# Performance work log

Hardware: AMD Instinct MI355X
Metric: run time of the kernel (lower is better)

The kernel has to match this reference:

```python
import jax, jax.numpy as jnp
import numpy as np

M = 30000      # total nodes
D = 64         # hidden_channels
B = 256        # number of graphs
E = 480000     # number of edges
NUM_ITER = 3   # Newton-Schulz iterations
EPS_TRIU = 0.001  # fix_triu diagonal jitter


def setup_inputs() -> dict:
    key = jax.random.key(0)
    k1, k2, k3 = jax.random.split(key, 3)
    x = jax.random.normal(k1, (M, D), dtype=jnp.float32)
    # sorted segment ids, every graph non-empty (sorted_randint semantics)
    batch = ((jnp.arange(M) * B) // M).astype(jnp.int32)
    edge = jax.random.randint(k2, (2, E), 0, M)
    W_att = jax.random.normal(k3, (D * D, 1), dtype=jnp.float32) / D
    b_att = jnp.zeros((1,), dtype=jnp.float32)
    return {"x": x, "batch": batch, "edge": edge, "W_att": W_att, "b_att": b_att}


def _segment_softmax(v, seg, num_segments):
    # v: [M], seg: [M] -> per-segment softmax
    m = jax.ops.segment_max(v, seg, num_segments=num_segments)
    e = jnp.exp(v - m[seg])
    s = jax.ops.segment_sum(e, seg, num_segments=num_segments)
    return e / s[seg]


def _sqrtm_ns(A, n_iter):
    # Newton-Schulz iterative matrix square root (MPN-COV Sqrtm)
    d = A.shape[-1]
    I = jnp.eye(d, dtype=A.dtype)
    normA = jnp.trace(A, axis1=-2, axis2=-1)[:, None, None]  # [B,1,1]
    Y = A / normA
    Z = jnp.broadcast_to(I, A.shape)
    for _ in range(n_iter):
        T = 0.5 * (3.0 * I - jnp.matmul(Z, Y))
        Y = jnp.matmul(Y, T)
        Z = jnp.matmul(T, Z)
    return Y * jnp.sqrt(normA)


def reference(x, batch, edge, W_att, b_att):
    Mn, Dd = x.shape
    # per-node outer products: einsum 'ik,kj->kij' on (x^T, x)
    wj = x[:, :, None] * x[:, None, :]              # [M, D, D]
    flat = wj.reshape(Mn, Dd * Dd)                  # [M, D*D]
    imp = (flat @ W_att + b_att)[:, 0]              # [M]
    imp = _segment_softmax(imp, batch, B)[:, None]  # scatter_softmax
    # scatter_mean(imp * flat, batch)
    num = jax.ops.segment_sum(imp * flat, batch, num_segments=B)
    cnt = jax.ops.segment_sum(jnp.ones((Mn,), x.dtype), batch, num_segments=B)
    out = (num / jnp.maximum(cnt, 1.0)[:, None]).reshape(B, Dd, Dd)
    # fix_triu: add eps * I before matrix sqrt
    out = out + EPS_TRIU * jnp.eye(Dd, dtype=out.dtype)
    out = _sqrtm_ns(out, NUM_ITER)
    # Triuvec: upper triangle incl. diagonal
    iu, ju = jnp.triu_indices(Dd)
    out = out[:, iu, ju]                            # [B, D*(D+1)/2]
    return out.reshape(B, -1)
```

## Files before the change

### kernel.cpp

```cpp
#include <hip/hip_runtime.h>
#include <math.h>

#define MN       30000
#define BSEG     256
#define EPS_TRIU 0.001f

#define XR_H 0
#define XR_L 8192
#define XT_H 16384
#define XT_L 24576
#define WT_H 32768
#define WT_L 36864
#define P_H 0
#define P_L 4096
#define Q_H 8192
#define Q_L 12288
#define R_H 16384
#define R_L 20480
#define S_H 24576
#define S_L 28672
#define V_H 32768
#define V_L 36864
#define IMP_F 20480
#define SWG_F 20608
#define SCL_F 20736
#define LDS_F4 5185

typedef __attribute__((ext_vector_type(8))) short bf16x8;
typedef __attribute__((ext_vector_type(4))) float f32x4;
#define MFMA_BF16(a, b, c) __builtin_amdgcn_mfma_f32_16x16x32_bf16(a, b, c, 0, 0, 0)

__device__ __forceinline__ float bf2f(short s) {
  return __uint_as_float(((unsigned)(unsigned short)s) << 16);
}
__device__ __forceinline__ void split2(float val, unsigned short& h, unsigned short& l) {
  const unsigned u = __float_as_uint(val);
  h = (unsigned short)(u >> 16);
  const float lo = val - __uint_as_float(u & 0xFFFF0000u);
  l = (unsigned short)(__float_as_uint(lo) >> 16);
}
__device__ __forceinline__ int sw64(int r, int c) { return (r << 6) + (c ^ ((r & 7) << 3)); }
__device__ __forceinline__ int sw128(int r, int c) { return (r << 7) + (c ^ ((r & 15) << 3)); }

template <int EPIT>
__device__ __forceinline__ void mm8(unsigned short* U, int dh, int dl,
                                    int ah_, int al_, int bh_, int bl_,
                                    int w, int r16, int kq) {
  const int mb = w >> 1;
  const int nb0 = (w & 1) << 1;
  const int ra = (mb << 4) + r16;
  const int mB = (mb << 4) + (kq << 2);
  bf16x8 Ah[2], Al[2];
#pragma unroll
  for (int ks = 0; ks < 2; ++ks) {
    const int ia = sw64(ra, (ks << 5) + (kq << 3));
    Ah[ks] = *(const bf16x8*)(U + ah_ + ia);
    Al[ks] = *(const bf16x8*)(U + al_ + ia);
  }
#pragma unroll
  for (int h = 0; h < 2; ++h) {
    const int nr = ((nb0 + h) << 4) + r16;
    bf16x8 Bh[2], Bl[2];
#pragma unroll
    for (int ks = 0; ks < 2; ++ks) {
      const int ib = sw64(nr, (ks << 5) + (kq << 3));
      Bh[ks] = *(const bf16x8*)(U + bh_ + ib);
      Bl[ks] = *(const bf16x8*)(U + bl_ + ib);
    }
    f32x4 acc = (f32x4)0.0f;
#pragma unroll
    for (int ks = 0; ks < 2; ++ks) {
      acc = MFMA_BF16(Ah[ks], Bh[ks], acc);
      acc = MFMA_BF16(Ah[ks], Bl[ks], acc);
      acc = MFMA_BF16(Al[ks], Bh[ks], acc);
    }
    short4 h4, l4;
#pragma unroll
    for (int e = 0; e < 4; ++e) {
      float v = acc[e];
      if (EPIT) v = -0.5f * v + ((mB + e) == nr ? 1.5f : 0.0f);
      unsigned short hh, ll;
      split2(v, hh, ll);
      ((unsigned short*)&h4)[e] = hh;
      ((unsigned short*)&l4)[e] = ll;
    }
    const int id = sw64(nr, mB);
    *(short4*)(U + dh + id) = h4;
    *(short4*)(U + dl + id) = l4;
  }
}

__device__ __forceinline__ void mm8_y3(unsigned short* U, int ah_, int al_,
                                       int bh_, int bl_, int w, float scale,
                                       float* __restrict__ ob, int r16, int kq) {
  const int mb = w >> 1;
  const int nb0 = (w & 1) << 1;
  if (mb > nb0 + 1) return;
  const int ra = (mb << 4) + r16;
  const int mB = (mb << 4) + (kq << 2);
  bf16x8 Ah[2], Al[2];
#pragma unroll
  for (int ks = 0; ks < 2; ++ks) {
    const int ia = sw64(ra, (ks << 5) + (kq << 3));
    Ah[ks] = *(const bf16x8*)(U + ah_ + ia);
    Al[ks] = *(const bf16x8*)(U + al_ + ia);
  }
#pragma unroll
  for (int h = 0; h < 2; ++h) {
    const int nb = nb0 + h;
    if (mb > nb) continue;
    const int nr = (nb << 4) + r16;
    bf16x8 Bh[2], Bl[2];
#pragma unroll
    for (int ks = 0; ks < 2; ++ks) {
      const int ib = sw64(nr, (ks << 5) + (kq << 3));
      Bh[ks] = *(const bf16x8*)(U + bh_ + ib);
      Bl[ks] = *(const bf16x8*)(U + bl_ + ib);
    }
    f32x4 acc = (f32x4)0.0f;
#pragma unroll
    for (int ks = 0; ks < 2; ++ks) {
      acc = MFMA_BF16(Ah[ks], Bh[ks], acc);
      acc = MFMA_BF16(Ah[ks], Bl[ks], acc);
      acc = MFMA_BF16(Al[ks], Bh[ks], acc);
    }
#pragma unroll
    for (int e = 0; e < 4; ++e) {
      const int m = mB + e;
      if (m <= nr) ob[((m * (129 - m)) >> 1) + nr - m] = acc[e] * scale;
    }
  }
}

template <int EPIT>
__device__ __forceinline__ void mm4(unsigned short* U, int dh, int dl,
                                    int ah_, int al_, int bh_, int bl_,
                                    int mq, int nq, int r16, int kq) {
  bf16x8 Ah[2][2], Al[2][2], Bh[2][2], Bl[2][2];
#pragma unroll
  for (int blk = 0; blk < 2; ++blk) {
    const int ra = (mq << 5) + (blk << 4) + r16;
    const int rb = (nq << 5) + (blk << 4) + r16;
#pragma unroll
    for (int ks = 0; ks < 2; ++ks) {
      const int co = (ks << 5) + (kq << 3);
      const int ia = sw64(ra, co), ib = sw64(rb, co);
      Ah[blk][ks] = *(const bf16x8*)(U + ah_ + ia);
      Al[blk][ks] = *(const bf16x8*)(U + al_ + ia);
      Bh[blk][ks] = *(const bf16x8*)(U + bh_ + ib);
      Bl[blk][ks] = *(const bf16x8*)(U + bl_ + ib);
    }
  }
#pragma unroll
  for (int mb = 0; mb < 2; ++mb)
#pragma unroll
    for (int nb = 0; nb < 2; ++nb) {
      f32x4 acc = (f32x4)0.0f;
#pragma unroll
      for (int ks = 0; ks < 2; ++ks) {
        acc = MFMA_BF16(Ah[mb][ks], Bh[nb][ks], acc);
        acc = MFMA_BF16(Ah[mb][ks], Bl[nb][ks], acc);
        acc = MFMA_BF16(Al[mb][ks], Bh[nb][ks], acc);
      }
      const int nr = (nq << 5) + (nb << 4) + r16;
      const int mB = (mq << 5) + (mb << 4) + (kq << 2);
      short4 h4, l4;
#pragma unroll
      for (int e = 0; e < 4; ++e) {
        float v = acc[e];
        if (EPIT) v = -0.5f * v + ((mB + e) == nr ? 1.5f : 0.0f);
        unsigned short hh, ll;
        split2(v, hh, ll);
        ((unsigned short*)&h4)[e] = hh;
        ((unsigned short*)&l4)[e] = ll;
      }
      const int id = sw64(nr, mB);
      *(short4*)(U + dh + id) = h4;
      *(short4*)(U + dl + id) = l4;
    }
}

extern "C" __global__ __launch_bounds__(512, 1) void readout_fused(
    const float* __restrict__ x, const float* __restrict__ Watt, float* __restrict__ out) {
  __shared__ float4 lds4[LDS_F4];
  float* ldsf = (float*)lds4;
  unsigned short* U = (unsigned short*)lds4;

  const int b = blockIdx.x;
  const int t = threadIdx.x;
  const int w = t >> 6, lane = t & 63;
  const int r16 = lane & 15, kq = lane >> 4;
  const int start = (b * MN + BSEG - 1) / BSEG;
  const int end = ((b + 1) * MN + BSEG - 1) / BSEG;
  const int n = end - start;

  const float4* W4 = (const float4*)Watt;
  const float4* X4 = (const float4*)x;

  if (t == 0) ldsf[SCL_F] = 0.0f;
  const bool doW = (t < 256);
  const int kt = t >> 4, nt = t & 15;
  float4 gw[4];
  if (doW) {
#pragma unroll
    for (int i = 0; i < 4; ++i) gw[i] = W4[((kt << 2) + i) * 16 + nt];
  }
  {
    const int jt = t >> 4, dt = t & 15;
    const int j4 = jt << 2, d4 = dt << 2;
    float4 g[4];
#pragma unroll
    for (int i = 0; i < 4; ++i)
      g[i] = (j4 + i < n) ? X4[(size_t)(start + j4 + i) * 16 + dt]
                          : make_float4(0.f, 0.f, 0.f, 0.f);
    unsigned short hs[4][4], ls[4][4];
#pragma unroll
    for (int i = 0; i < 4; ++i)
#pragma unroll
      for (int e = 0; e < 4; ++e) split2((&g[i].x)[e], hs[i][e], ls[i][e]);
#pragma unroll
    for (int i = 0; i < 4; ++i) {
      short4 h4, l4;
#pragma unroll
      for (int e = 0; e < 4; ++e) {
        ((unsigned short*)&h4)[e] = hs[i][e];
        ((unsigned short*)&l4)[e] = ls[i][e];
      }
      const int ir = sw64(j4 + i, d4);
      *(short4*)(U + XR_H + ir) = h4;
      *(short4*)(U + XR_L + ir) = l4;
    }
#pragma unroll
    for (int e = 0; e < 4; ++e) {
      short4 h4, l4;
#pragma unroll
      for (int i = 0; i < 4; ++i) {
        ((unsigned short*)&h4)[i] = hs[i][e];
        ((unsigned short*)&l4)[i] = ls[i][e];
      }
      const int it = sw128(d4 + e, j4);
      *(short4*)(U + XT_H + it) = h4;
      *(short4*)(U + XT_L + it) = l4;
    }
  }
  if (doW) {
    const int k4 = kt << 2, n4 = nt << 2;
#pragma unroll
    for (int e = 0; e < 4; ++e) {
      short4 h4, l4;
#pragma unroll
      for (int i = 0; i < 4; ++i) {
        unsigned short hh, ll;
        split2((&gw[i].x)[e], hh, ll);
        ((unsigned short*)&h4)[i] = hh;
        ((unsigned short*)&l4)[i] = ll;
      }
      const int idx = sw64(n4 + e, k4);
      *(short4*)(U + WT_H + idx) = h4;
      *(short4*)(U + WT_L + idx) = l4;
    }
  }
  __syncthreads();

  {
    const int jrow = (w << 4) + r16;
    bf16x8 Bh[2], Bl[2];
#pragma unroll
    for (int ks = 0; ks < 2; ++ks) {
      const int ib = sw64(jrow, (ks << 5) + (kq << 3));
      Bh[ks] = *(const bf16x8*)(U + XR_H + ib);
      Bl[ks] = *(const bf16x8*)(U + XR_L + ib);
    }
    float partial = 0.0f;
#pragma unroll
    for (int mb = 0; mb < 4; ++mb) {
      bf16x8 Ah[2], Al[2];
#pragma unroll
      for (int ks = 0; ks < 2; ++ks) {
        const int ia = sw64((mb << 4) + r16, (ks << 5) + (kq << 3));
        Ah[ks] = *(const bf16x8*)(U + WT_H + ia);
        Al[ks] = *(const bf16x8*)(U + WT_L + ia);
      }
      f32x4 acc = (f32x4)0.0f;
#pragma unroll
      for (int ks = 0; ks < 2; ++ks) {
        acc = MFMA_BF16(Ah[ks], Bh[ks], acc);
        acc = MFMA_BF16(Ah[ks], Bl[ks], acc);
        acc = MFMA_BF16(Al[ks], Bh[ks], acc);
      }
      const int xi = sw64(jrow, (mb << 4) + (kq << 2));
      const short4 xh = *(const short4*)(U + XR_H + xi);
      const short4 xl = *(const short4*)(U + XR_L + xi);
#pragma unroll
      for (int e = 0; e < 4; ++e)
        partial += acc[e] * (bf2f(((const short*)&xh)[e]) + bf2f(((const short*)&xl)[e]));
    }
    partial += __shfl_xor(partial, 16, 64);
    partial += __shfl_xor(partial, 32, 64);
    if (kq == 0) ldsf[IMP_F + jrow] = partial;
  }
  __syncthreads();

  bf16x8 pxh0 = *(const bf16x8*)(U + XT_H + t * 8);
  bf16x8 pxl0 = *(const bf16x8*)(U + XT_L + t * 8);
  bf16x8 pxh1 = *(const bf16x8*)(U + XT_H + (t + 512) * 8);
  bf16x8 pxl1 = *(const bf16x8*)(U + XT_L + (t + 512) * 8);
  if (t < 64) {
    float v0 = (t < n) ? ldsf[IMP_F + t] : -3.0e38f;
    float v1 = (t + 64 < n) ? ldsf[IMP_F + t + 64] : -3.0e38f;
    float m = fmaxf(v0, v1);
#pragma unroll
    for (int s = 32; s; s >>= 1) m = fmaxf(m, __shfl_xor(m, s, 64));
    float e0 = (t < n) ? expf(v0 - m) : 0.0f;
    float e1 = (t + 64 < n) ? expf(v1 - m) : 0.0f;
    float se = e0 + e1;
#pragma unroll
    for (int s = 32; s; s >>= 1) se += __shfl_xor(se, s, 64);
    const float inv = 1.0f / (se * (float)n);
    ldsf[SWG_F + t] = sqrtf(e0 * inv);
    ldsf[SWG_F + t + 64] = sqrtf(e1 * inv);
  }
  __syncthreads();

  {
    float ss = 0.0f;
#pragma unroll
    for (int g = 0; g < 2; ++g) {
      const int v = t + (g << 9);
      const int d = v >> 4;
      const int j0 = ((v & 15) << 3) ^ ((d & 15) << 3);
      bf16x8 hh = g ? pxh1 : pxh0;
      bf16x8 ll = g ? pxl1 : pxl0;
#pragma unroll
      for (int e = 0; e < 8; ++e) {
        const float val = (bf2f(hh[e]) + bf2f(ll[e])) * ldsf[SWG_F + j0 + e];
        ss = fmaf(val, val, ss);
        unsigned short nh, nl;
        split2(val, nh, nl);
        hh[e] = (short)nh;
        ll[e] = (short)nl;
      }
      *(bf16x8*)(U + XT_H + v * 8) = hh;
      *(bf16x8*)(U + XT_L + v * 8) = ll;
    }
#pragma unroll
    for (int s = 1; s <= 32; s <<= 1) ss += __shfl_xor(ss, s, 64);
    if (lane == 0) atomicAdd(&ldsf[SCL_F], ss);
  }
  __syncthreads();

  const float normA = ldsf[SCL_F] + 64.0f * EPS_TRIU;
  const float rn = 1.0f / normA;
  const float scale = sqrtf(normA);

  if (w < 4) {
    const int mq = w >> 1, nq = w & 1;
    bf16x8 Ah[2][4], Al[2][4];
#pragma unroll
    for (int mb = 0; mb < 2; ++mb) {
      const int ra = (mq << 5) + (mb << 4) + r16;
#pragma unroll
      for (int ks = 0; ks < 4; ++ks) {
        const int ia = sw128(ra, (ks << 5) + (kq << 3));
        Ah[mb][ks] = *(const bf16x8*)(U + XT_H + ia);
        Al[mb][ks] = *(const bf16x8*)(U + XT_L + ia);
      }
    }
#pragma unroll
    for (int nb = 0; nb < 2; ++nb) {
      const int nr = (nq << 5) + (nb << 4) + r16;
      bf16x8 Bh[4], Bl[4];
      if (mq == nq) {
#pragma unroll
        for (int ks = 0; ks < 4; ++ks) { Bh[ks] = Ah[nb][ks]; Bl[ks] = Al[nb][ks]; }
      } else {
#pragma unroll
        for (int ks = 0; ks < 4; ++ks) {
          const int ib = sw128(nr, (ks << 5) + (kq << 3));
          Bh[ks] = *(const bf16x8*)(U + XT_H + ib);
          Bl[ks] = *(const bf16x8*)(U + XT_L + ib);
        }
      }
#pragma unroll
      for (int mb = 0; mb < 2; ++mb) {
        f32x4 acc = (f32x4)0.0f;
#pragma unroll
        for (int ks = 0; ks < 4; ++ks) {
          acc = MFMA_BF16(Ah[mb][ks], Bh[ks], acc);
          acc = MFMA_BF16(Ah[mb][ks], Bl[ks], acc);
          acc = MFMA_BF16(Al[mb][ks], Bh[ks], acc);
        }
        const int mB = (mq << 5) + (mb << 4) + (kq << 2);
        short4 yh, yl, th, tl;
#pragma unroll
        for (int e = 0; e < 4; ++e) {
          const int diag = ((mB + e) == nr);
          const float a = acc[e] + (diag ? EPS_TRIU : 0.0f);
          const float y = a * rn;
          unsigned short hh, ll;
          split2(y, hh, ll);
          ((unsigned short*)&yh)[e] = hh;
          ((unsigned short*)&yl)[e] = ll;
          const float tv = (diag ? 1.5f : 0.0f) - 0.5f * y;
          split2(tv, hh, ll);
          ((unsigned short*)&th)[e] = hh;
          ((unsigned short*)&tl)[e] = ll;
        }
        const int id = sw64(nr, mB);
        *(short4*)(U + P_H + id) = yh;
        *(short4*)(U + P_L + id) = yl;
        *(short4*)(U + V_H + id) = th;
        *(short4*)(U + V_L + id) = tl;
      }
    }
  }
  __syncthreads();

  mm8<0>(U, Q_H, Q_L, P_H, P_L, V_H, V_L, w, r16, kq);
  __syncthreads();
  mm8<1>(U, S_H, S_L, V_H, V_L, Q_H, Q_L, w, r16, kq);
  __syncthreads();
  if (w < 4)
    mm4<0>(U, R_H, R_L, Q_H, Q_L, S_H, S_L, w >> 1, w & 1, r16, kq);
  else
    mm4<0>(U, P_H, P_L, S_H, S_L, V_H, V_L, (w - 4) >> 1, (w - 4) & 1, r16, kq);
  __syncthreads();
  mm8<1>(U, V_H, V_L, P_H, P_L, R_H, R_L, w, r16, kq);
  __syncthreads();
  mm8_y3(U, R_H, R_L, V_H, V_L, w, scale, out + (size_t)b * 2080, r16, kq);
}

extern "C" void kernel_launch(void* const* d_in, const int* in_sizes, int n_in,
                              void* d_out, int out_size, void* d_ws, size_t ws_size,
                              hipStream_t stream) {
  const float* x = (const float*)d_in[0];
  const float* Watt = (const float*)d_in[3];
  float* out = (float*)d_out;
  readout_fused<<<dim3(BSEG), dim3(512), 0, stream>>>(x, Watt, out);
}
```

Measured before the change: 14.98 us.

## Compute softmax weights redundantly per wave and split Gram matmul across all eight waves

Every wave now computes the segment softmax max and sum itself and derives its own eight per-column weights in registers. This removes the LDS round trip of the weight array and one block-wide barrier, and switches to the fast __expf. The X^T X Gram stage, which only four waves ran before, is now split across all eight waves, each computing two 16x16 output tiles. The cost is redundant exp and shuffle-reduction work in every wave and slightly lower exp accuracy.

After: 15.14 us. About the same (+1.0%).

```diff
diff --git a/kernel.cpp b/kernel.cpp
--- a/kernel.cpp
+++ b/kernel.cpp
@@ -22,9 +22,8 @@
 #define V_H 32768
 #define V_L 36864
 #define IMP_F 20480
-#define SWG_F 20608
-#define SCL_F 20736
-#define LDS_F4 5185
+#define SCL_F 20608
+#define LDS_F4 5153
 
 typedef __attribute__((ext_vector_type(8))) short bf16x8;
 typedef __attribute__((ext_vector_type(4))) float f32x4;
@@ -301,45 +300,46 @@
   }
   __syncthreads();
 
-  bf16x8 pxh0 = *(const bf16x8*)(U + XT_H + t * 8);
-  bf16x8 pxl0 = *(const bf16x8*)(U + XT_L + t * 8);
-  bf16x8 pxh1 = *(const bf16x8*)(U + XT_H + (t + 512) * 8);
-  bf16x8 pxl1 = *(const bf16x8*)(U + XT_L + (t + 512) * 8);
-  if (t < 64) {
-    float v0 = (t < n) ? ldsf[IMP_F + t] : -3.0e38f;
-    float v1 = (t + 64 < n) ? ldsf[IMP_F + t + 64] : -3.0e38f;
+  {
+    bf16x8 pxh0 = *(const bf16x8*)(U + XT_H + t * 8);
+    bf16x8 pxl0 = *(const bf16x8*)(U + XT_L + t * 8);
+    bf16x8 pxh1 = *(const bf16x8*)(U + XT_H + (t + 512) * 8);
+    bf16x8 pxl1 = *(const bf16x8*)(U + XT_L + (t + 512) * 8);
+    const int j0 = ((t & 15) << 3) ^ (((t >> 4) & 15) << 3);
+    const float4 ia4 = *(const float4*)(ldsf + IMP_F + j0);
+    const float4 ib4 = *(const float4*)(ldsf + IMP_F + j0 + 4);
+    float v0 = (lane < n) ? ldsf[IMP_F + lane] : -3.0e38f;
+    float v1 = (lane + 64 < n) ? ldsf[IMP_F + lane + 64] : -3.0e38f;
     float m = fmaxf(v0, v1);
 #pragma unroll
     for (int s = 32; s; s >>= 1) m = fmaxf(m, __shfl_xor(m, s, 64));
-    float e0 = (t < n) ? expf(v0 - m) : 0.0f;
-    float e1 = (t + 64 < n) ? expf(v1 - m) : 0.0f;
+    float e0 = (lane < n) ? __expf(v0 - m) : 0.0f;
+    float e1 = (lane + 64 < n) ? __expf(v1 - m) : 0.0f;
     float se = e0 + e1;
 #pragma unroll
     for (int s = 32; s; s >>= 1) se += __shfl_xor(se, s, 64);
     const float inv = 1.0f / (se * (float)n);
-    ldsf[SWG_F + t] = sqrtf(e0 * inv);
-    ldsf[SWG_F + t + 64] = sqrtf(e1 * inv);
-  }
-  __syncthreads();
-
-  {
+    float s8[8];
+#pragma unroll
+    for (int e = 0; e < 8; ++e) {
+      const float impv = (e < 4) ? (&ia4.x)[e] : (&ib4.x)[e - 4];
+      s8[e] = sqrtf(__expf(impv - m) * inv);
+    }
     float ss = 0.0f;
 #pragma unroll
     for (int g = 0; g < 2; ++g) {
-      const int v = t + (g << 9);
-      const int d = v >> 4;
-      const int j0 = ((v & 15) << 3) ^ ((d & 15) << 3);
       bf16x8 hh = g ? pxh1 : pxh0;
       bf16x8 ll = g ? pxl1 : pxl0;
 #pragma unroll
       for (int e = 0; e < 8; ++e) {
-        const float val = (bf2f(hh[e]) + bf2f(ll[e])) * ldsf[SWG_F + j0 + e];
+        const float val = (bf2f(hh[e]) + bf2f(ll[e])) * s8[e];
         ss = fmaf(val, val, ss);
         unsigned short nh, nl;
         split2(val, nh, nl);
         hh[e] = (short)nh;
         ll[e] = (short)nl;
       }
+      const int v = t + (g << 9);
       *(bf16x8*)(U + XT_H + v * 8) = hh;
       *(bf16x8*)(U + XT_L + v * 8) = ll;
     }
@@ -353,65 +353,66 @@
   const float rn = 1.0f / normA;
   const float scale = sqrtf(normA);
 
-  if (w < 4) {
-    const int mq = w >> 1, nq = w & 1;
+  {
+    const int mb0 = (w >> 2) << 1;
+    const int nb = w & 3;
+    const int nr = (nb << 4) + r16;
     bf16x8 Ah[2][4], Al[2][4];
 #pragma unroll
-    for (int mb = 0; mb < 2; ++mb) {
-      const int ra = (mq << 5) + (mb << 4) + r16;
+    for (int mi = 0; mi < 2; ++mi) {
+      const int ra = ((mb0 + mi) << 4) + r16;
 #pragma unroll
       for (int ks = 0; ks < 4; ++ks) {
         const int ia = sw128(ra, (ks << 5) + (kq << 3));
-        Ah[mb][ks] = *(const bf16x8*)(U + XT_H + ia);
-        Al[mb][ks] = *(const bf16x8*)(U + XT_L + ia);
-      }
-    }
-#pragma unroll
-    for (int nb = 0; nb < 2; ++nb) {
-      const int nr = (nq << 5) + (nb << 4) + r16;
-      bf16x8 Bh[4], Bl[4];
-      if (mq == nq) {
-#pragma unroll
-        for (int ks = 0; ks < 4; ++ks) { Bh[ks] = Ah[nb][ks]; Bl[ks] = Al[nb][ks]; }
-      } else {
-#pragma unroll
-        for (int ks = 0; ks < 4; ++ks) {
-          const int ib = sw128(nr, (ks << 5) + (kq << 3));
-          Bh[ks] = *(const bf16x8*)(U + XT_H + ib);
-          Bl[ks] = *(const bf16x8*)(U + XT_L + ib);
-        }
-      }
-#pragma unroll
-      for (int mb = 0; mb < 2; ++mb) {
-        f32x4 acc = (f32x4)0.0f;
-#pragma unroll
-        for (int ks = 0; ks < 4; ++ks) {
-          acc = MFMA_BF16(Ah[mb][ks], Bh[ks], acc);
-          acc = MFMA_BF16(Ah[mb][ks], Bl[ks], acc);
-          acc = MFMA_BF16(Al[mb][ks], Bh[ks], acc);
-        }
-        const int mB = (mq << 5) + (mb << 4) + (kq << 2);
-        short4 yh, yl, th, tl;
-#pragma unroll
-        for (int e = 0; e < 4; ++e) {
-          const int diag = ((mB + e) == nr);
-          const float a = acc[e] + (diag ? EPS_TRIU : 0.0f);
-          const float y = a * rn;
-          unsigned short hh, ll;
-          split2(y, hh, ll);
-          ((unsigned short*)&yh)[e] = hh;
-          ((unsigned short*)&yl)[e] = ll;
-          const float tv = (diag ? 1.5f : 0.0f) - 0.5f * y;
-          split2(tv, hh, ll);
-          ((unsigned short*)&th)[e] = hh;
-          ((unsigned short*)&tl)[e] = ll;
-        }
-        const int id = sw64(nr, mB);
-        *(short4*)(U + P_H + id) = yh;
-        *(short4*)(U + P_L + id) = yl;
-        *(short4*)(U + V_H + id) = th;
-        *(short4*)(U + V_L + id) = tl;
-      }
+        Ah[mi][ks] = *(const bf16x8*)(U + XT_H + ia);
+        Al[mi][ks] = *(const bf16x8*)(U + XT_L + ia);
+      }
+    }
+    bf16x8 Bh[4], Bl[4];
+    if (nb == mb0) {
+#pragma unroll
+      for (int ks = 0; ks < 4; ++ks) { Bh[ks] = Ah[0][ks]; Bl[ks] = Al[0][ks]; }
+    } else if (nb == mb0 + 1) {
+#pragma unroll
+      for (int ks = 0; ks < 4; ++ks) { Bh[ks] = Ah[1][ks]; Bl[ks] = Al[1][ks]; }
+    } else {
+#pragma unroll
+      for (int ks = 0; ks < 4; ++ks) {
+        const int ib = sw128(nr, (ks << 5) + (kq << 3));
+        Bh[ks] = *(const bf16x8*)(U + XT_H + ib);
+        Bl[ks] = *(const bf16x8*)(U + XT_L + ib);
+      }
+    }
+#pragma unroll
+    for (int mi = 0; mi < 2; ++mi) {
+      f32x4 acc = (f32x4)0.0f;
+#pragma unroll
+      for (int ks = 0; ks < 4; ++ks) {
+        acc = MFMA_BF16(Ah[mi][ks], Bh[ks], acc);
+        acc = MFMA_BF16(Ah[mi][ks], Bl[ks], acc);
+        acc = MFMA_BF16(Al[mi][ks], Bh[ks], acc);
+      }
+      const int mB = ((mb0 + mi) << 4) + (kq << 2);
+      short4 yh, yl, th, tl;
+#pragma unroll
+      for (int e = 0; e < 4; ++e) {
+        const int diag = ((mB + e) == nr);
+        const float a = acc[e] + (diag ? EPS_TRIU : 0.0f);
+        const float y = a * rn;
+        unsigned short hh, ll;
+        split2(y, hh, ll);
+        ((unsigned short*)&yh)[e] = hh;
+        ((unsigned short*)&yl)[e] = ll;
+        const float tv = (diag ? 1.5f : 0.0f) - 0.5f * y;
+        split2(tv, hh, ll);
+        ((unsigned short*)&th)[e] = hh;
+        ((unsigned short*)&tl)[e] = ll;
+      }
+      const int id = sw64(nr, mB);
+      *(short4*)(U + P_H + id) = yh;
+      *(short4*)(U + P_L + id) = yl;
+      *(short4*)(U + V_H + id) = th;
+      *(short4*)(U + V_L + id) = tl;
     }
   }
   __syncthreads();
```
